# Performance work log

Measured on AMD Instinct MI355X. Metric: run time of the kernel, lower is better.

Reference implementation:

```python
import jax, jax.numpy as jnp
import numpy as np

DIM_E, DIM_M, DIM_C = 1024, 64, 128
B, N = 4, 4096


def setup_inputs() -> dict:
    key = jax.random.key(0)
    ks = jax.random.split(key, 10)
    s = 1.0 / np.sqrt(DIM_E + DIM_C)
    return {
        "e": jax.random.normal(ks[0], (B, N, DIM_E), jnp.float32),
        "m": jax.random.normal(ks[1], (B, N, DIM_M), jnp.float32),
        "c": jax.random.normal(ks[2], (B, N, DIM_C), jnp.float32),
        "l": jax.random.uniform(ks[3], (B, N), jnp.float32),
        "Wq": jax.random.uniform(ks[4], (DIM_E + DIM_C, DIM_E), jnp.float32, -s, s),
        "bq": jax.random.uniform(ks[5], (DIM_E,), jnp.float32, -s, s),
        "Wk": jax.random.uniform(ks[6], (DIM_E + DIM_C, DIM_E), jnp.float32, -s, s),
        "bk": jax.random.uniform(ks[7], (DIM_E,), jnp.float32, -s, s),
        "Wv": jax.random.uniform(ks[8], (DIM_E + DIM_C, DIM_E), jnp.float32, -s, s),
        "bv": jax.random.uniform(ks[9], (DIM_E,), jnp.float32, -s, s),
    }


def reference(e, m, c, l, Wq, bq, Wk, bk, Wv, bv):
    x = jnp.concatenate([e, c], axis=-1)                       # [B,N,De+Dc]
    q = jnp.einsum('bnd,df->bnf', x, Wq) + bq                  # [B,N,De]
    k = jnp.einsum('bnd,df->bnf', x, Wk) + bk
    v = jnp.einsum('bnd,df->bnf', x, Wv) + bv
    scale = 1.0 / jnp.sqrt(jnp.asarray(q.shape[-1], q.dtype))
    attn_scores = jnp.einsum('bqd,bkd->bqk', q, k) * scale     # [B,N,N]
    membrane_mask = jnp.einsum('bqm,bkm->bqk', m, m)           # [B,N,N]
    lifespan_mask = l[:, :, None] * l[:, None, :]              # [B,N,N]
    adaptive_scores = attn_scores * membrane_mask * lifespan_mask
    attn_weights = jax.nn.softmax(adaptive_scores, axis=-1)
    h_tilde = jnp.einsum('bqk,bkd->bqd', attn_weights, v)      # [B,N,De]
    e_new = e + h_tilde
    return (e_new, h_tilde)
```

## Files before the change

kernel.cpp:

```cpp
#include <hip/hip_runtime.h>
#include <hip/hip_bf16.h>

#define DE 1024
#define DM 64
#define DC 128
#define DX 1152
#define NB 4
#define NN 4096
#define NT 16384

typedef _Float16 f16;
typedef _Float16 f16x4 __attribute__((ext_vector_type(4)));
typedef _Float16 f16x8 __attribute__((ext_vector_type(8)));
typedef float f32x4 __attribute__((ext_vector_type(4)));

__device__ __forceinline__ void g2l16(const void* g, void* l) {
  __builtin_amdgcn_global_load_lds(
      (const __attribute__((address_space(1))) unsigned int*)(unsigned long long)g,
      (__attribute__((address_space(3))) unsigned int*)(unsigned int)(unsigned long long)l,
      16, 0, 0);
}

#define SBAR() do { __builtin_amdgcn_sched_barrier(0);                 \
                    __builtin_amdgcn_s_barrier();                      \
                    __builtin_amdgcn_sched_barrier(0); } while (0)
#define VMWAIT(n) do { __builtin_amdgcn_sched_barrier(0);              \
                       asm volatile("s_waitcnt vmcnt(" #n ")");        \
                       __builtin_amdgcn_sched_barrier(0); } while (0)
#define LGKM0() do { __builtin_amdgcn_sched_barrier(0);                \
                     asm volatile("s_waitcnt lgkmcnt(0)");             \
                     __builtin_amdgcn_sched_barrier(0); } while (0)

__global__ void build_x_kernel(const float* __restrict__ e, const float* __restrict__ c,
                               f16* __restrict__ Xb) {
  const int total = NT * DX / 4;
  for (int i = blockIdx.x * blockDim.x + threadIdx.x; i < total; i += gridDim.x * blockDim.x) {
    int idx = i * 4;
    int r = idx / DX, col = idx - r * DX;
    float4 v;
    if (col < DE) v = *(const float4*)(e + (long)r * DE + col);
    else          v = *(const float4*)(c + (long)r * DC + (col - DE));
    f16x4 o = { (f16)v.x, (f16)v.y, (f16)v.z, (f16)v.w };
    *(f16x4*)(Xb + (long)idx) = o;
  }
}

__global__ void conv_f16_kernel(const float* __restrict__ in, f16* __restrict__ out, int total4) {
  for (int i = blockIdx.x * blockDim.x + threadIdx.x; i < total4; i += gridDim.x * blockDim.x) {
    float4 v = *(const float4*)(in + (long)i * 4);
    f16x4 o = { (f16)v.x, (f16)v.y, (f16)v.z, (f16)v.w };
    *(f16x4*)(out + (long)i * 4) = o;
  }
}

__global__ void transpose_w_kernel(const float* __restrict__ in, f16* __restrict__ out) {
  __shared__ float tile[32][33];
  int c0 = blockIdx.x * 32, r0 = blockIdx.y * 32;
  int x = threadIdx.x, y = threadIdx.y;
#pragma unroll
  for (int i = 0; i < 4; ++i)
    tile[y + 8 * i][x] = in[(long)(r0 + y + 8 * i) * DE + (c0 + x)];
  __syncthreads();
#pragma unroll
  for (int i = 0; i < 4; ++i)
    out[(long)(c0 + y + 8 * i) * DX + (r0 + x)] = (f16)tile[x][y + 8 * i];
}

__device__ __forceinline__ void mm_loop(const f16* __restrict__ A, const f16* __restrict__ B,
                                        int lda, int ldb, int K,
                                        f16* lA, f16* lB, f32x4 (&acc)[4][4]) {
  const int t = threadIdx.x;
  const int lane = t & 63;
  const int wid = t >> 6;
  const int wr = (wid >> 1) * 64, wc = (wid & 1) * 64;
  const int fr = lane & 15, fq = lane >> 4;
  for (int k0 = 0; k0 < K; k0 += 32) {
    __syncthreads();
#pragma unroll
    for (int it = 0; it < 2; ++it) {
      int byteoff = it * 4096 + t * 16;
      int row = byteoff >> 6;
      int ke = (byteoff & 63) >> 1;
      g2l16(A + (long)row * lda + k0 + ke, lA + (byteoff >> 1));
      g2l16(B + (long)row * ldb + k0 + ke, lB + (byteoff >> 1));
    }
    __syncthreads();
    f16x8 af[4], bfr[4];
#pragma unroll
    for (int i = 0; i < 4; ++i) {
      af[i]  = *(const f16x8*)(lA + (wr + i * 16 + fr) * 32 + fq * 8);
      bfr[i] = *(const f16x8*)(lB + (wc + i * 16 + fr) * 32 + fq * 8);
    }
#pragma unroll
    for (int m = 0; m < 4; ++m)
#pragma unroll
      for (int n = 0; n < 4; ++n)
        acc[m][n] = __builtin_amdgcn_mfma_f32_16x16x32_f16(af[m], bfr[n], acc[m][n], 0, 0, 0);
  }
}

__global__ __launch_bounds__(256) void mask_kernel(
    const f16* __restrict__ mb, const float* __restrict__ l, f16* __restrict__ Pm) {
  __shared__ __attribute__((aligned(16))) f16 lA[128 * 32], lB[128 * 32];
  f32x4 acc[4][4];
#pragma unroll
  for (int m = 0; m < 4; ++m)
#pragma unroll
    for (int n = 0; n < 4; ++n) acc[m][n] = (f32x4){0.f, 0.f, 0.f, 0.f};
  const int b = blockIdx.z;
  const int row0 = blockIdx.x * 128, col0 = blockIdx.y * 128;
  mm_loop(mb + (long)(b * NN + row0) * DM, mb + (long)(b * NN + col0) * DM,
          DM, DM, DM, lA, lB, acc);
  const int lane = threadIdx.x & 63, wid = threadIdx.x >> 6;
  const int wr = (wid >> 1) * 64, wc = (wid & 1) * 64;
  const int fr = lane & 15, fq = lane >> 4;
  const float* lb = l + (long)b * NN;
  f16* out = Pm + (long)b * NN * NN;
#pragma unroll
  for (int n = 0; n < 4; ++n) {
    int col = col0 + wc + n * 16 + fr;
    float lc = lb[col] * 0.03125f;
#pragma unroll
    for (int m = 0; m < 4; ++m)
#pragma unroll
      for (int r = 0; r < 4; ++r) {
        int row = row0 + wr + m * 16 + fq * 4 + r;
        out[(long)row * NN + col] = (f16)(acc[m][n][r] * lc * lb[row]);
      }
  }
}

__device__ __forceinline__ void gemm4_core(
    const f16* __restrict__ A, long lda,
    const f16* __restrict__ B, long ldb,
    int NTt, char* ldsb, f32x4 (&acc)[8][4]) {
  const int tid = threadIdx.x;
  const int lane = tid & 63, wid = tid >> 6;
  const int wr = wid >> 1, wc = wid & 1;
  const int fr = lane & 15, fq = lane >> 4;

  const f16* srcA = A + (long)(tid >> 2) * lda + (tid & 3) * 8;
  const f16* srcB = B + (long)(tid >> 2) * ldb + (tid & 3) * 8;

  auto stageA = [&](int kt, int par) {
    char* base = ldsb + par * 24576;
#pragma unroll
    for (int it = 0; it < 4; ++it)
      g2l16(srcA + (long)(it * 64) * lda + kt * 32, base + it * 4096 + tid * 16);
  };
  auto stageB = [&](int kt, int par) {
    char* base = ldsb + par * 24576 + 16384;
#pragma unroll
    for (int it = 0; it < 2; ++it)
      g2l16(srcB + (long)(it * 64) * ldb + kt * 32, base + it * 4096 + tid * 16);
  };

  const int aoff = (wr * 128 + fr) * 64 + fq * 16;
  const int boff = (wc * 64 + fr) * 64 + fq * 16;

  auto mma16 = [&](f16x8 (&a4)[4], f16x8 (&b4)[4], int mo) {
    __builtin_amdgcn_s_setprio(1);
#pragma unroll
    for (int m = 0; m < 4; ++m)
#pragma unroll
      for (int n = 0; n < 4; ++n)
        acc[mo + m][n] =
            __builtin_amdgcn_mfma_f32_16x16x32_f16(a4[m], b4[n], acc[mo + m][n], 0, 0, 0);
    __builtin_amdgcn_s_setprio(0);
  };

  stageA(0, 0); stageB(0, 0); stageA(1, 1); stageB(1, 1);
  VMWAIT(6);
  SBAR();

  for (int tt = 0; tt < NTt; ++tt) {
    const int par = tt & 1;
    const char* bA = ldsb + par * 24576;
    const char* bB = bA + 16384;
    f16x8 af[4], af2[4], bf[4];
#pragma unroll
    for (int i = 0; i < 4; ++i)
      af[i] = *(const f16x8*)(const void*)(bA + aoff + i * 1024);
#pragma unroll
    for (int n = 0; n < 4; ++n)
      bf[n] = *(const f16x8*)(const void*)(bB + boff + n * 1024);
    mma16(af, bf, 0);
#pragma unroll
    for (int i = 0; i < 4; ++i)
      af2[i] = *(const f16x8*)(const void*)(bA + aoff + 4096 + i * 1024);
    LGKM0();
    SBAR();
    mma16(af2, bf, 4);
    if (tt + 2 < NTt) {
      stageA(tt + 2, par); stageB(tt + 2, par);
      VMWAIT(6);
    } else {
      VMWAIT(0);
    }
    SBAR();
  }
}

__device__ __forceinline__ void swz_grid(int& bx, int& by, int& bz) {
  int nx = gridDim.x, ny = gridDim.y;
  int flat = blockIdx.x + nx * (blockIdx.y + ny * blockIdx.z);
  int total = nx * ny * gridDim.z;
  int cpx = total >> 3;
  flat = (flat & 7) * cpx + (flat >> 3);
  bx = flat % nx; int r = flat / nx;
  by = r % ny; bz = r / ny;
}

#define ACC_INIT()                                                  \
  f32x4 acc[8][4];                                                  \
  _Pragma("unroll") for (int m_ = 0; m_ < 8; ++m_)                  \
  _Pragma("unroll") for (int n_ = 0; n_ < 4; ++n_)                  \
      acc[m_][n_] = (f32x4){0.f, 0.f, 0.f, 0.f};

#define EPI4_IDX()                                                  \
  const int lane = threadIdx.x & 63, wid = threadIdx.x >> 6;        \
  const int wr = wid >> 1, wc = wid & 1;                            \
  const int fr = lane & 15, fq = lane >> 4;

__global__ __launch_bounds__(256, 2) void qk8_kernel(
    const f16* __restrict__ Xb, const f16* __restrict__ Wt,
    const float* __restrict__ bq, const float* __restrict__ bk,
    f16* __restrict__ qb, f16* __restrict__ kb) {
  __shared__ __attribute__((aligned(128))) char ldsb[49152];
  int bx, by, bz; swz_grid(bx, by, bz);
  const int row0 = bx * 256, col0 = by * 128;
  ACC_INIT();
  gemm4_core(Xb + (long)row0 * DX, DX, Wt + (long)col0 * DX, DX, DX / 32, ldsb, acc);
  EPI4_IDX();
  const bool isq = col0 < DE;
  const float* bvec = isq ? bq : bk;
  f16* ob = isq ? qb : kb;
  const int cbase = (isq ? col0 : col0 - DE) + wc * 64;
  const int rbase = row0 + wr * 128;
#pragma unroll
  for (int n = 0; n < 4; ++n) {
    int col = cbase + n * 16 + fr;
    float bb = bvec[col];
#pragma unroll
    for (int m = 0; m < 8; ++m)
#pragma unroll
      for (int j = 0; j < 4; ++j) {
        int row = rbase + m * 16 + fq * 4 + j;
        ob[(long)row * DE + col] = (f16)(acc[m][n][j] + bb);
      }
  }
}

__global__ __launch_bounds__(256, 2) void vt8_kernel(
    const f16* __restrict__ WtV, const f16* __restrict__ Xb,
    const float* __restrict__ bv, f16* __restrict__ Vt) {
  __shared__ __attribute__((aligned(128))) char ldsb[49152];
  int bx, by, bz; swz_grid(bx, by, bz);
  const int row0 = bx * 256, col0 = by * 128;
  ACC_INIT();
  gemm4_core(WtV + (long)row0 * DX, DX, Xb + (long)col0 * DX, DX, DX / 32, ldsb, acc);
  EPI4_IDX();
  const int cbase = col0 + wc * 64;
  const int rbase = row0 + wr * 128;
#pragma unroll
  for (int n = 0; n < 4; ++n) {
    int col = cbase + n * 16 + fr;
#pragma unroll
    for (int m = 0; m < 8; ++m)
#pragma unroll
      for (int j = 0; j < 4; ++j) {
        int row = rbase + m * 16 + fq * 4 + j;
        Vt[(long)row * NT + col] = (f16)(acc[m][n][j] + bv[row]);
      }
  }
}

__global__ __launch_bounds__(256, 2) void sc8_kernel(
    const f16* __restrict__ qb_, const f16* __restrict__ kb_, float* __restrict__ S) {
  __shared__ __attribute__((aligned(128))) char ldsb[49152];
  int bx, by, bz; swz_grid(bx, by, bz);
  const int row0 = bx * 256, col0 = by * 128;
  ACC_INIT();
  gemm4_core(qb_ + (long)row0 * DE, DE, kb_ + (long)col0 * DE, DE, DE / 32, ldsb, acc);
  EPI4_IDX();
  const int cbase = col0 + wc * 64;
  const int rbase = row0 + wr * 128;
#pragma unroll
  for (int n = 0; n < 4; ++n) {
    int col = cbase + n * 16 + fr;
#pragma unroll
    for (int m = 0; m < 8; ++m)
#pragma unroll
      for (int j = 0; j < 4; ++j) {
        int row = rbase + m * 16 + fq * 4 + j;
        S[(long)row * NN + col] = acc[m][n][j];
      }
  }
}

__global__ __launch_bounds__(256, 2) void pv8_kernel(
    const f16* __restrict__ P, const f16* __restrict__ Vt,
    const float* __restrict__ e, float* __restrict__ outE, float* __restrict__ outH) {
  __shared__ __attribute__((aligned(128))) char ldsb[49152];
  int bx, by, bz; swz_grid(bx, by, bz);
  const int b = bz;
  const int row0 = bx * 256, col0 = by * 128;
  ACC_INIT();
  gemm4_core(P + (long)b * NN * NN + (long)row0 * NN, NN,
             Vt + (long)col0 * NT + (long)b * NN, NT, NN / 32, ldsb, acc);
  EPI4_IDX();
  const int cbase = col0 + wc * 64;
  const int rbase = row0 + wr * 128;
#pragma unroll
  for (int n = 0; n < 4; ++n) {
    int col = cbase + n * 16 + fr;
#pragma unroll
    for (int m = 0; m < 8; ++m)
#pragma unroll
      for (int j = 0; j < 4; ++j) {
        int row = rbase + m * 16 + fq * 4 + j;
        long idx = ((long)b * NN + row) * DE + col;
        float h = acc[m][n][j];
        outE[idx] = e[idx] + h;
        outH[idx] = h;
      }
  }
}

__global__ __launch_bounds__(256) void softmax_kernel(const float* __restrict__ S,
                                                      const f16* __restrict__ Pm,
                                                      f16* __restrict__ P) {
  __shared__ float red[8];
  const long row = blockIdx.x;
  const float* s = S + row * NN;
  const f16* pmr = Pm + row * NN;
  const int t = threadIdx.x;
  float4 v[4];
  float mx = -3.0e38f;
#pragma unroll
  for (int i = 0; i < 4; ++i) {
    v[i] = *(const float4*)(s + t * 4 + i * 1024);
    f16x4 m4 = *(const f16x4*)(pmr + t * 4 + i * 1024);
    v[i].x *= (float)m4[0]; v[i].y *= (float)m4[1];
    v[i].z *= (float)m4[2]; v[i].w *= (float)m4[3];
    mx = fmaxf(mx, fmaxf(fmaxf(v[i].x, v[i].y), fmaxf(v[i].z, v[i].w)));
  }
#pragma unroll
  for (int o = 32; o; o >>= 1) mx = fmaxf(mx, __shfl_xor(mx, o));
  if ((t & 63) == 0) red[t >> 6] = mx;
  __syncthreads();
  mx = fmaxf(fmaxf(red[0], red[1]), fmaxf(red[2], red[3]));
  float sum = 0.f;
#pragma unroll
  for (int i = 0; i < 4; ++i) {
    v[i].x = __expf(v[i].x - mx); v[i].y = __expf(v[i].y - mx);
    v[i].z = __expf(v[i].z - mx); v[i].w = __expf(v[i].w - mx);
    sum += v[i].x + v[i].y + v[i].z + v[i].w;
  }
#pragma unroll
  for (int o = 32; o; o >>= 1) sum += __shfl_xor(sum, o);
  if ((t & 63) == 0) red[4 + (t >> 6)] = sum;
  __syncthreads();
  float inv = 1.f / (red[4] + red[5] + red[6] + red[7]);
  f16* p = P + row * NN;
#pragma unroll
  for (int i = 0; i < 4; ++i) {
    f16x4 o4 = { (f16)(v[i].x * inv), (f16)(v[i].y * inv),
                 (f16)(v[i].z * inv), (f16)(v[i].w * inv) };
    *(f16x4*)(p + t * 4 + i * 1024) = o4;
  }
}

extern "C" void kernel_launch(void* const* d_in, const int* in_sizes, int n_in,
                              void* d_out, int out_size, void* d_ws, size_t ws_size,
                              hipStream_t stream) {
  const float* e  = (const float*)d_in[0];
  const float* m  = (const float*)d_in[1];
  const float* c  = (const float*)d_in[2];
  const float* l  = (const float*)d_in[3];
  const float* Wq = (const float*)d_in[4];
  const float* bq = (const float*)d_in[5];
  const float* Wk = (const float*)d_in[6];
  const float* bk = (const float*)d_in[7];
  const float* Wv = (const float*)d_in[8];
  const float* bv = (const float*)d_in[9];
  float* outE = (float*)d_out;
  float* outH = outE + (long)NT * DE;

  char* ws = (char*)d_ws;
  size_t off = 0;
  auto alloc = [&](size_t bytes) {
    char* p = ws + off;
    off += (bytes + 255) & ~(size_t)255;
    return p;
  };
  f16* Xb    = (f16*)alloc((size_t)NT * DX * 2);
  f16* WtQK  = (f16*)alloc((size_t)2048 * DX * 2);
  f16* WtV   = (f16*)alloc((size_t)DE * DX * 2);
  f16* qb    = (f16*)alloc((size_t)NT * DE * 2);
  f16* kb    = (f16*)alloc((size_t)NT * DE * 2);
  f16* Vt    = (f16*)alloc((size_t)DE * NT * 2);
  f16* mb    = (f16*)alloc((size_t)NT * DM * 2);
  float* S   = (float*)alloc((size_t)NN * NN * 4);
  f16* P     = (f16*)alloc((size_t)NB * NN * NN * 2);
  if (off > ws_size) return;

  build_x_kernel<<<2048, 256, 0, stream>>>(e, c, Xb);
  conv_f16_kernel<<<512, 256, 0, stream>>>(m, mb, NT * DM / 4);
  transpose_w_kernel<<<dim3(32, 36), dim3(32, 8), 0, stream>>>(Wq, WtQK);
  transpose_w_kernel<<<dim3(32, 36), dim3(32, 8), 0, stream>>>(Wk, WtQK + (size_t)DE * DX);
  transpose_w_kernel<<<dim3(32, 36), dim3(32, 8), 0, stream>>>(Wv, WtV);
  mask_kernel<<<dim3(32, 32, NB), 256, 0, stream>>>(mb, l, P);
  qk8_kernel<<<dim3(64, 16), 256, 0, stream>>>(Xb, WtQK, bq, bk, qb, kb);
  vt8_kernel<<<dim3(4, 128), 256, 0, stream>>>(WtV, Xb, bv, Vt);
  for (int b = 0; b < NB; ++b) {
    sc8_kernel<<<dim3(16, 32), 256, 0, stream>>>(
        qb + (size_t)b * NN * DE, kb + (size_t)b * NN * DE, S);
    softmax_kernel<<<NN, 256, 0, stream>>>(S, P + (size_t)b * NN * NN, P + (size_t)b * NN * NN);
  }
  pv8_kernel<<<dim3(16, 8, NB), 256, 0, stream>>>(P, Vt, e, outE, outH);
}
```

Baseline: 782.9 us.

## Rework GEMM core to 128x128x64 tiles with XOR-swizzled LDS

Replaces the shared GEMM core, shrinking each block tile from 256x128 to 128x128 and deepening the K step from 32 to 64. The core now uses a simple double-buffered prefetch-next-then-compute loop with __syncthreads instead of hand-tuned waitcnt and sched barriers. An XOR swizzle on the LDS layout is added to avoid bank conflicts on fragment reads. Grids double in the tiled dimension, which gives more blocks for occupancy but halves per-block reuse, grows LDS to 64KB per block, and drops the finer-grained overlap of the previous pipeline.

```diff
diff --git a/kernel.cpp b/kernel.cpp
--- a/kernel.cpp
+++ b/kernel.cpp
@@ -20,16 +20,6 @@
       (__attribute__((address_space(3))) unsigned int*)(unsigned int)(unsigned long long)l,
       16, 0, 0);
 }
-
-#define SBAR() do { __builtin_amdgcn_sched_barrier(0);                 \
-                    __builtin_amdgcn_s_barrier();                      \
-                    __builtin_amdgcn_sched_barrier(0); } while (0)
-#define VMWAIT(n) do { __builtin_amdgcn_sched_barrier(0);              \
-                       asm volatile("s_waitcnt vmcnt(" #n ")");        \
-                       __builtin_amdgcn_sched_barrier(0); } while (0)
-#define LGKM0() do { __builtin_amdgcn_sched_barrier(0);                \
-                     asm volatile("s_waitcnt lgkmcnt(0)");             \
-                     __builtin_amdgcn_sched_barrier(0); } while (0)
 
 __global__ void build_x_kernel(const float* __restrict__ e, const float* __restrict__ c,
                                f16* __restrict__ Xb) {
@@ -133,71 +123,61 @@
 __device__ __forceinline__ void gemm4_core(
     const f16* __restrict__ A, long lda,
     const f16* __restrict__ B, long ldb,
-    int NTt, char* ldsb, f32x4 (&acc)[8][4]) {
+    int NTt, char* ldsb, f32x4 (&acc)[4][4]) {
   const int tid = threadIdx.x;
   const int lane = tid & 63, wid = tid >> 6;
   const int wr = wid >> 1, wc = wid & 1;
   const int fr = lane & 15, fq = lane >> 4;
-
-  const f16* srcA = A + (long)(tid >> 2) * lda + (tid & 3) * 8;
-  const f16* srcB = B + (long)(tid >> 2) * ldb + (tid & 3) * 8;
-
-  auto stageA = [&](int kt, int par) {
-    char* base = ldsb + par * 24576;
-#pragma unroll
-    for (int it = 0; it < 4; ++it)
-      g2l16(srcA + (long)(it * 64) * lda + kt * 32, base + it * 4096 + tid * 16);
+  const int cb0 = ((fq) ^ (fr & 7)) << 4;
+  const int cb1 = ((4 | fq) ^ (fr & 7)) << 4;
+
+  auto stage = [&](const f16* __restrict__ S, long ld, int kt, char* base) {
+#pragma unroll
+    for (int it = 0; it < 4; ++it) {
+      int off = it * 4096 + tid * 16;
+      int sw = off ^ (((off >> 7) & 7) << 4);
+      int row = sw >> 7;
+      int colf = ((sw >> 4) & 7) << 3;
+      g2l16(S + (long)row * ld + kt * 64 + colf, base + off);
+    }
   };
-  auto stageB = [&](int kt, int par) {
-    char* base = ldsb + par * 24576 + 16384;
-#pragma unroll
-    for (int it = 0; it < 2; ++it)
-      g2l16(srcB + (long)(it * 64) * ldb + kt * 32, base + it * 4096 + tid * 16);
-  };
-
-  const int aoff = (wr * 128 + fr) * 64 + fq * 16;
-  const int boff = (wc * 64 + fr) * 64 + fq * 16;
-
-  auto mma16 = [&](f16x8 (&a4)[4], f16x8 (&b4)[4], int mo) {
-    __builtin_amdgcn_s_setprio(1);
-#pragma unroll
-    for (int m = 0; m < 4; ++m)
-#pragma unroll
-      for (int n = 0; n < 4; ++n)
-        acc[mo + m][n] =
-            __builtin_amdgcn_mfma_f32_16x16x32_f16(a4[m], b4[n], acc[mo + m][n], 0, 0, 0);
-    __builtin_amdgcn_s_setprio(0);
-  };
-
-  stageA(0, 0); stageB(0, 0); stageA(1, 1); stageB(1, 1);
-  VMWAIT(6);
-  SBAR();
+
+  stage(A, lda, 0, ldsb);
+  stage(B, ldb, 0, ldsb + 16384);
+  __syncthreads();
 
   for (int tt = 0; tt < NTt; ++tt) {
     const int par = tt & 1;
-    const char* bA = ldsb + par * 24576;
-    const char* bB = bA + 16384;
-    f16x8 af[4], af2[4], bf[4];
-#pragma unroll
-    for (int i = 0; i < 4; ++i)
-      af[i] = *(const f16x8*)(const void*)(bA + aoff + i * 1024);
-#pragma unroll
-    for (int n = 0; n < 4; ++n)
-      bf[n] = *(const f16x8*)(const void*)(bB + boff + n * 1024);
-    mma16(af, bf, 0);
-#pragma unroll
-    for (int i = 0; i < 4; ++i)
-      af2[i] = *(const f16x8*)(const void*)(bA + aoff + 4096 + i * 1024);
-    LGKM0();
-    SBAR();
-    mma16(af2, bf, 4);
-    if (tt + 2 < NTt) {
-      stageA(tt + 2, par); stageB(tt + 2, par);
-      VMWAIT(6);
-    } else {
-      VMWAIT(0);
-    }
-    SBAR();
+    const char* cur = ldsb + par * 32768;
+    char* nxt = ldsb + (par ^ 1) * 32768;
+    if (tt + 1 < NTt) {
+      stage(A, lda, tt + 1, nxt);
+      stage(B, ldb, tt + 1, nxt + 16384);
+    }
+    __builtin_amdgcn_sched_barrier(0);
+    f16x8 a[4][2], b[4][2];
+#pragma unroll
+    for (int i = 0; i < 4; ++i) {
+      int row = wr * 64 + i * 16 + fr;
+      a[i][0] = *(const f16x8*)(const void*)(cur + row * 128 + cb0);
+      a[i][1] = *(const f16x8*)(const void*)(cur + row * 128 + cb1);
+    }
+#pragma unroll
+    for (int i = 0; i < 4; ++i) {
+      int row = wc * 64 + i * 16 + fr;
+      b[i][0] = *(const f16x8*)(const void*)(cur + 16384 + row * 128 + cb0);
+      b[i][1] = *(const f16x8*)(const void*)(cur + 16384 + row * 128 + cb1);
+    }
+    __builtin_amdgcn_s_setprio(1);
+#pragma unroll
+    for (int k = 0; k < 2; ++k)
+#pragma unroll
+      for (int m = 0; m < 4; ++m)
+#pragma unroll
+        for (int n = 0; n < 4; ++n)
+          acc[m][n] = __builtin_amdgcn_mfma_f32_16x16x32_f16(a[m][k], b[n][k], acc[m][n], 0, 0, 0);
+    __builtin_amdgcn_s_setprio(0);
+    __syncthreads();
   }
 }
 
@@ -212,8 +192,8 @@
 }
 
 #define ACC_INIT()                                                  \
-  f32x4 acc[8][4];                                                  \
-  _Pragma("unroll") for (int m_ = 0; m_ < 8; ++m_)                  \
+  f32x4 acc[4][4];                                                  \
+  _Pragma("unroll") for (int m_ = 0; m_ < 4; ++m_)                  \
   _Pragma("unroll") for (int n_ = 0; n_ < 4; ++n_)                  \
       acc[m_][n_] = (f32x4){0.f, 0.f, 0.f, 0.f};
 
@@ -226,23 +206,23 @@
     const f16* __restrict__ Xb, const f16* __restrict__ Wt,
     const float* __restrict__ bq, const float* __restrict__ bk,
     f16* __restrict__ qb, f16* __restrict__ kb) {
-  __shared__ __attribute__((aligned(128))) char ldsb[49152];
+  __shared__ __attribute__((aligned(128))) char ldsb[65536];
   int bx, by, bz; swz_grid(bx, by, bz);
-  const int row0 = bx * 256, col0 = by * 128;
+  const int row0 = bx * 128, col0 = by * 128;
   ACC_INIT();
-  gemm4_core(Xb + (long)row0 * DX, DX, Wt + (long)col0 * DX, DX, DX / 32, ldsb, acc);
+  gemm4_core(Xb + (long)row0 * DX, DX, Wt + (long)col0 * DX, DX, DX / 64, ldsb, acc);
   EPI4_IDX();
   const bool isq = col0 < DE;
   const float* bvec = isq ? bq : bk;
   f16* ob = isq ? qb : kb;
   const int cbase = (isq ? col0 : col0 - DE) + wc * 64;
-  const int rbase = row0 + wr * 128;
+  const int rbase = row0 + wr * 64;
 #pragma unroll
   for (int n = 0; n < 4; ++n) {
     int col = cbase + n * 16 + fr;
     float bb = bvec[col];
 #pragma unroll
-    for (int m = 0; m < 8; ++m)
+    for (int m = 0; m < 4; ++m)
 #pragma unroll
       for (int j = 0; j < 4; ++j) {
         int row = rbase + m * 16 + fq * 4 + j;
@@ -254,19 +234,19 @@
 __global__ __launch_bounds__(256, 2) void vt8_kernel(
     const f16* __restrict__ WtV, const f16* __restrict__ Xb,
     const float* __restrict__ bv, f16* __restrict__ Vt) {
-  __shared__ __attribute__((aligned(128))) char ldsb[49152];
+  __shared__ __attribute__((aligned(128))) char ldsb[65536];
   int bx, by, bz; swz_grid(bx, by, bz);
-  const int row0 = bx * 256, col0 = by * 128;
+  const int row0 = bx * 128, col0 = by * 128;
   ACC_INIT();
-  gemm4_core(WtV + (long)row0 * DX, DX, Xb + (long)col0 * DX, DX, DX / 32, ldsb, acc);
+  gemm4_core(WtV + (long)row0 * DX, DX, Xb + (long)col0 * DX, DX, DX / 64, ldsb, acc);
   EPI4_IDX();
   const int cbase = col0 + wc * 64;
-  const int rbase = row0 + wr * 128;
+  const int rbase = row0 + wr * 64;
 #pragma unroll
   for (int n = 0; n < 4; ++n) {
     int col = cbase + n * 16 + fr;
 #pragma unroll
-    for (int m = 0; m < 8; ++m)
+    for (int m = 0; m < 4; ++m)
 #pragma unroll
       for (int j = 0; j < 4; ++j) {
         int row = rbase + m * 16 + fq * 4 + j;
@@ -277,19 +257,19 @@
 
 __global__ __launch_bounds__(256, 2) void sc8_kernel(
     const f16* __restrict__ qb_, const f16* __restrict__ kb_, float* __restrict__ S) {
-  __shared__ __attribute__((aligned(128))) char ldsb[49152];
+  __shared__ __attribute__((aligned(128))) char ldsb[65536];
   int bx, by, bz; swz_grid(bx, by, bz);
-  const int row0 = bx * 256, col0 = by * 128;
+  const int row0 = bx * 128, col0 = by * 128;
   ACC_INIT();
-  gemm4_core(qb_ + (long)row0 * DE, DE, kb_ + (long)col0 * DE, DE, DE / 32, ldsb, acc);
+  gemm4_core(qb_ + (long)row0 * DE, DE, kb_ + (long)col0 * DE, DE, DE / 64, ldsb, acc);
   EPI4_IDX();
   const int cbase = col0 + wc * 64;
-  const int rbase = row0 + wr * 128;
+  const int rbase = row0 + wr * 64;
 #pragma unroll
   for (int n = 0; n < 4; ++n) {
     int col = cbase + n * 16 + fr;
 #pragma unroll
-    for (int m = 0; m < 8; ++m)
+    for (int m = 0; m < 4; ++m)
 #pragma unroll
       for (int j = 0; j < 4; ++j) {
         int row = rbase + m * 16 + fq * 4 + j;
@@ -301,21 +281,21 @@
 __global__ __launch_bounds__(256, 2) void pv8_kernel(
     const f16* __restrict__ P, const f16* __restrict__ Vt,
     const float* __restrict__ e, float* __restrict__ outE, float* __restrict__ outH) {
-  __shared__ __attribute__((aligned(128))) char ldsb[49152];
+  __shared__ __attribute__((aligned(128))) char ldsb[65536];
   int bx, by, bz; swz_grid(bx, by, bz);
   const int b = bz;
-  const int row0 = bx * 256, col0 = by * 128;
+  const int row0 = bx * 128, col0 = by * 128;
   ACC_INIT();
   gemm4_core(P + (long)b * NN * NN + (long)row0 * NN, NN,
-             Vt + (long)col0 * NT + (long)b * NN, NT, NN / 32, ldsb, acc);
+             Vt + (long)col0 * NT + (long)b * NN, NT, NN / 64, ldsb, acc);
   EPI4_IDX();
   const int cbase = col0 + wc * 64;
-  const int rbase = row0 + wr * 128;
+  const int rbase = row0 + wr * 64;
 #pragma unroll
   for (int n = 0; n < 4; ++n) {
     int col = cbase + n * 16 + fr;
 #pragma unroll
-    for (int m = 0; m < 8; ++m)
+    for (int m = 0; m < 4; ++m)
 #pragma unroll
       for (int j = 0; j < 4; ++j) {
         int row = rbase + m * 16 + fq * 4 + j;
@@ -411,12 +391,12 @@
   transpose_w_kernel<<<dim3(32, 36), dim3(32, 8), 0, stream>>>(Wk, WtQK + (size_t)DE * DX);
   transpose_w_kernel<<<dim3(32, 36), dim3(32, 8), 0, stream>>>(Wv, WtV);
   mask_kernel<<<dim3(32, 32, NB), 256, 0, stream>>>(mb, l, P);
-  qk8_kernel<<<dim3(64, 16), 256, 0, stream>>>(Xb, WtQK, bq, bk, qb, kb);
-  vt8_kernel<<<dim3(4, 128), 256, 0, stream>>>(WtV, Xb, bv, Vt);
+  qk8_kernel<<<dim3(128, 16), 256, 0, stream>>>(Xb, WtQK, bq, bk, qb, kb);
+  vt8_kernel<<<dim3(8, 128), 256, 0, stream>>>(WtV, Xb, bv, Vt);
   for (int b = 0; b < NB; ++b) {
-    sc8_kernel<<<dim3(16, 32), 256, 0, stream>>>(
+    sc8_kernel<<<dim3(32, 32), 256, 0, stream>>>(
         qb + (size_t)b * NN * DE, kb + (size_t)b * NN * DE, S);
     softmax_kernel<<<NN, 256, 0, stream>>>(S, P + (size_t)b * NN * NN, P + (size_t)b * NN * NN);
   }
-  pv8_kernel<<<dim3(16, 8, NB), 256, 0, stream>>>(P, Vt, e, outE, outH);
-}
+  pv8_kernel<<<dim3(32, 8, NB), 256, 0, stream>>>(P, Vt, e, outE, outH);
+}
```

Measured after the change: 739.5 us. 5.5% less time.
